# Kernel tuning notes

Measured on AMD Instinct MI355X. Metric: run time of the kernel, lower is better.

## Reference

```python
import jax, jax.numpy as jnp
import numpy as np

NUM_BINS = 32
FAIRNESS_PENALTY = 0.1
SENSITIVE = (0, 5)


def setup_inputs() -> dict:
    key = jax.random.key(0)
    k1, k2, k3, k4 = jax.random.split(key, 4)
    B, F, P = 65536, 256, 32
    x = jax.random.uniform(k1, (B, F), dtype=jnp.float32)  # features in [0,1)
    W = jax.random.normal(k2, (F, NUM_BINS), dtype=jnp.float32) * 0.1  # main-effect weights
    IW = jax.random.normal(k3, (P, NUM_BINS, NUM_BINS), dtype=jnp.float32) * 0.1  # pairwise weights
    intercept = jax.random.normal(k4, (1,), dtype=jnp.float32)
    # build(): feature_bins[i] = linspace(0, 1, num_bins+1) for every feature
    bins = jnp.tile(jnp.linspace(0.0, 1.0, NUM_BINS + 1, dtype=jnp.float32)[None, :], (F, 1))
    pair_i = jnp.arange(P, dtype=jnp.int32) * 2  # interaction_terms = [(0,1),(2,3),...]
    pair_j = pair_i + 1
    return dict(x=x, W=W, IW=IW, intercept=intercept, bins=bins, pair_i=pair_i, pair_j=pair_j)


def _bin_indices(x, bins):
    # x: [B,F], bins: [F,NB+1] -> int32 [B,F]; matches tf sum(x>=bins)-1 with clip
    idx = jnp.sum((x[:, :, None] >= bins[None, :, :]).astype(jnp.int32), axis=-1) - 1
    return jnp.clip(idx, 0, NUM_BINS - 1)


def reference(x, W, IW, intercept, bins, pair_i, pair_j):
    B, F = x.shape
    P = IW.shape[0]
    idx = _bin_indices(x, bins)  # [B,F]
    main = W[jnp.arange(F)[None, :], idx]  # per-feature gathered contributions [B,F]
    inter = IW[jnp.arange(P)[None, :], idx[:, pair_i], idx[:, pair_j]]  # [B,P]
    preds = intercept[0] + main.sum(axis=1) + inter.sum(axis=1)  # [B]
    fairness_loss = FAIRNESS_PENALTY * sum(jnp.var(main[:, s]) for s in SENSITIVE)
    return preds[:, None], fairness_loss
```

## Files before the change

### kernel.cpp

```cpp
#include <hip/hip_runtime.h>


#define F        256
#define NBINS    32
#define PPAIRS   32
#define WPB      8
#define BLOCK    (WPB * 64)
#define GRID     1024
#define WPAD     (NBINS + 1)

template <int ctrl, int row_mask, int bank_mask>
__device__ __forceinline__ float dpp_add(float x) {
    int y = __builtin_amdgcn_update_dpp(0, __float_as_int(x), ctrl, row_mask, bank_mask, false);
    return x + __int_as_float(y);
}

__device__ __forceinline__ float wave_sum_lane63(float x) {
    x = dpp_add<0x111, 0xf, 0xf>(x);
    x = dpp_add<0x112, 0xf, 0xf>(x);
    x = dpp_add<0x114, 0xf, 0xe>(x);
    x = dpp_add<0x118, 0xf, 0xc>(x);
    x = dpp_add<0x142, 0xa, 0xf>(x);
    x = dpp_add<0x143, 0x8, 0xf>(x);
    return x;
}

__global__ __launch_bounds__(BLOCK, 8) void febm_main(
    const float* __restrict__ x, const float* __restrict__ W,
    const float* __restrict__ IW, const float* __restrict__ intercept,
    float* __restrict__ out, float4* __restrict__ partials, int B)
{
    __shared__ float Wl[F * WPAD];
    __shared__ float4 mm[WPB];

    for (int i = threadIdx.x; i < F * NBINS; i += BLOCK) {
        int f = i >> 5, k = i & 31;
        Wl[f * WPAD + k] = W[i];
    }
    __syncthreads();

    const int lane = threadIdx.x & 63;
    const int wave = threadIdx.x >> 6;
    const int gw = blockIdx.x * WPB + wave;
    const int total_waves = GRID * WPB;
    const int rows_per_wave = B / total_waves;
    const int base = gw * rows_per_wave;

    const float c0 = intercept[0];

    float sA = 0.f, ssA = 0.f;

    const float4* xr = (const float4*)x;
    float4 xv = xr[(size_t)base * (F / 4) + lane];

    for (int r = 0; r < rows_per_wave; ++r) {
        const int b = base + r;
        float4 xnext;
        if (r + 1 < rows_per_wave)
            xnext = xr[(size_t)(b + 1) * (F / 4) + lane];

        float msum = 0.f, wf = 0.f;
        unsigned packed = 0;
        const float xe[4] = {xv.x, xv.y, xv.z, xv.w};
        #pragma unroll
        for (int i = 0; i < 4; ++i) {
            int k = (int)(xe[i] * 32.0f);
            k = k < 0 ? 0 : (k > NBINS - 1 ? NBINS - 1 : k);
            const int f = lane * 4 + i;
            const float w = Wl[f * WPAD + k];
            msum += w;
            packed |= (unsigned)k << (i * 8);
            if (i == 0) wf = w;
            if (i == 1 && lane == 1) wf = w;
        }

        const unsigned u = (unsigned)__shfl((int)packed, lane >> 1);
        float iv = 0.f;
        if (lane < PPAIRS) {
            const int sh = (lane & 1) * 16;
            const int ki = (u >> sh) & 0xff;
            const int kj = (u >> (sh + 8)) & 0xff;
            iv = IW[lane * (NBINS * NBINS) + ki * NBINS + kj];
        }

        const float tot = wave_sum_lane63(msum + iv);
        if (lane == 63) out[b] = c0 + tot;

        if (lane < 2) { sA += wf; ssA += wf * wf; }
        xv = xnext;
    }

    if (lane == 0) { mm[wave].x = sA; mm[wave].y = ssA; }
    if (lane == 1) { mm[wave].z = sA; mm[wave].w = ssA; }
    __syncthreads();
    if (threadIdx.x == 0) {
        float4 a = mm[0];
        #pragma unroll
        for (int w = 1; w < WPB; ++w) {
            a.x += mm[w].x; a.y += mm[w].y; a.z += mm[w].z; a.w += mm[w].w;
        }
        partials[blockIdx.x] = a;
    }
}

__global__ __launch_bounds__(256) void febm_reduce(
    const float4* __restrict__ partials, int nPart, float* __restrict__ fair_out, int B)
{
    __shared__ float4 sw[4];
    const int lane = threadIdx.x & 63;
    const int wave = threadIdx.x >> 6;

    float4 a = make_float4(0.f, 0.f, 0.f, 0.f);
    for (int i = threadIdx.x; i < nPart; i += 256) {
        const float4 p = partials[i];
        a.x += p.x; a.y += p.y; a.z += p.z; a.w += p.w;
    }
    #pragma unroll
    for (int off = 32; off > 0; off >>= 1) {
        a.x += __shfl_xor(a.x, off);
        a.y += __shfl_xor(a.y, off);
        a.z += __shfl_xor(a.z, off);
        a.w += __shfl_xor(a.w, off);
    }
    if (lane == 0) sw[wave] = a;
    __syncthreads();
    if (threadIdx.x == 0) {
        float4 t = sw[0];
        #pragma unroll
        for (int w = 1; w < 4; ++w) {
            t.x += sw[w].x; t.y += sw[w].y; t.z += sw[w].z; t.w += sw[w].w;
        }
        const double invB = 1.0 / (double)B;
        const double mean0 = t.x * invB, mean5 = t.z * invB;
        const double var0 = t.y * invB - mean0 * mean0;
        const double var5 = t.w * invB - mean5 * mean5;
        fair_out[0] = (float)(0.1 * (var0 + var5));
    }
}

extern "C" void kernel_launch(void* const* d_in, const int* in_sizes, int n_in,
                              void* d_out, int out_size, void* d_ws, size_t ws_size,
                              hipStream_t stream)
{
    const float* x         = (const float*)d_in[0];
    const float* W         = (const float*)d_in[1];
    const float* IW        = (const float*)d_in[2];
    const float* intercept = (const float*)d_in[3];

    float* out = (float*)d_out;
    const int B = in_sizes[0] / F;
    float4* partials = (float4*)d_ws;

    febm_main<<<GRID, BLOCK, 0, stream>>>(x, W, IW, intercept, out, partials, B);
    febm_reduce<<<1, 256, 0, stream>>>(partials, GRID, out + B, B);
}
```

Before: 116.9 us.

## Batch all per-wave row loads upfront and vectorize W staging and output stores

Each wave now issues all 8 of its row loads at once into registers, instead of a one-deep prefetch inside the loop. The per-row loop is fully unrolled with a fixed ROWS constant, and the 8 results are written as two float4 stores. W is staged into shared memory with float4 global loads, and the launch bound occupancy hint drops from 8 to 4. The aim is more memory-level parallelism for the 64 MB x stream, at the cost of higher register pressure. It also hardcodes B = GRID*WPB*ROWS, so other batch sizes would break.

```diff
diff --git a/kernel.cpp b/kernel.cpp
--- a/kernel.cpp
+++ b/kernel.cpp
@@ -7,6 +7,7 @@
 #define WPB      8
 #define BLOCK    (WPB * 64)
 #define GRID     1024
+#define ROWS     8
 #define WPAD     (NBINS + 1)
 
 template <int ctrl, int row_mask, int bank_mask>
@@ -25,69 +26,76 @@
     return x;
 }
 
-__global__ __launch_bounds__(BLOCK, 8) void febm_main(
+__global__ __launch_bounds__(BLOCK, 4) void febm_main(
     const float* __restrict__ x, const float* __restrict__ W,
     const float* __restrict__ IW, const float* __restrict__ intercept,
-    float* __restrict__ out, float4* __restrict__ partials, int B)
+    float* __restrict__ out, float4* __restrict__ partials)
 {
     __shared__ float Wl[F * WPAD];
     __shared__ float4 mm[WPB];
 
-    for (int i = threadIdx.x; i < F * NBINS; i += BLOCK) {
-        int f = i >> 5, k = i & 31;
-        Wl[f * WPAD + k] = W[i];
+    {
+        const float4* W4 = (const float4*)W;
+        for (int i = threadIdx.x; i < F * NBINS / 4; i += BLOCK) {
+            const float4 v = W4[i];
+            const int f = i >> 3, k4 = (i & 7) * 4;
+            float* dst = &Wl[f * WPAD + k4];
+            dst[0] = v.x; dst[1] = v.y; dst[2] = v.z; dst[3] = v.w;
+        }
     }
     __syncthreads();
 
     const int lane = threadIdx.x & 63;
     const int wave = threadIdx.x >> 6;
     const int gw = blockIdx.x * WPB + wave;
-    const int total_waves = GRID * WPB;
-    const int rows_per_wave = B / total_waves;
-    const int base = gw * rows_per_wave;
+    const int base = gw * ROWS;
 
     const float c0 = intercept[0];
 
+    const float4* xr = (const float4*)x;
+    float4 xv[ROWS];
+    #pragma unroll
+    for (int r = 0; r < ROWS; ++r)
+        xv[r] = xr[(size_t)(base + r) * (F / 4) + lane];
+
+    float msum[ROWS], iv[ROWS];
     float sA = 0.f, ssA = 0.f;
-
-    const float4* xr = (const float4*)x;
-    float4 xv = xr[(size_t)base * (F / 4) + lane];
-
-    for (int r = 0; r < rows_per_wave; ++r) {
-        const int b = base + r;
-        float4 xnext;
-        if (r + 1 < rows_per_wave)
-            xnext = xr[(size_t)(b + 1) * (F / 4) + lane];
-
-        float msum = 0.f, wf = 0.f;
+    #pragma unroll
+    for (int r = 0; r < ROWS; ++r) {
+        const float xe[4] = {xv[r].x, xv[r].y, xv[r].z, xv[r].w};
+        float acc = 0.f, wf = 0.f;
         unsigned packed = 0;
-        const float xe[4] = {xv.x, xv.y, xv.z, xv.w};
         #pragma unroll
         for (int i = 0; i < 4; ++i) {
             int k = (int)(xe[i] * 32.0f);
             k = k < 0 ? 0 : (k > NBINS - 1 ? NBINS - 1 : k);
-            const int f = lane * 4 + i;
-            const float w = Wl[f * WPAD + k];
-            msum += w;
+            const float w = Wl[(lane * 4 + i) * WPAD + k];
+            acc += w;
             packed |= (unsigned)k << (i * 8);
             if (i == 0) wf = w;
             if (i == 1 && lane == 1) wf = w;
         }
+        msum[r] = acc;
+        if (lane < 2) { sA += wf; ssA += wf * wf; }
 
         const unsigned u = (unsigned)__shfl((int)packed, lane >> 1);
-        float iv = 0.f;
+        float t = 0.f;
         if (lane < PPAIRS) {
             const int sh = (lane & 1) * 16;
             const int ki = (u >> sh) & 0xff;
             const int kj = (u >> (sh + 8)) & 0xff;
-            iv = IW[lane * (NBINS * NBINS) + ki * NBINS + kj];
+            t = IW[lane * (NBINS * NBINS) + ki * NBINS + kj];
         }
+        iv[r] = t;
+    }
 
-        const float tot = wave_sum_lane63(msum + iv);
-        if (lane == 63) out[b] = c0 + tot;
-
-        if (lane < 2) { sA += wf; ssA += wf * wf; }
-        xv = xnext;
+    float res[ROWS];
+    #pragma unroll
+    for (int r = 0; r < ROWS; ++r)
+        res[r] = c0 + wave_sum_lane63(msum[r] + iv[r]);
+    if (lane == 63) {
+        ((float4*)(out + base))[0] = make_float4(res[0], res[1], res[2], res[3]);
+        ((float4*)(out + base))[1] = make_float4(res[4], res[5], res[6], res[7]);
     }
 
     if (lane == 0) { mm[wave].x = sA; mm[wave].y = ssA; }
@@ -151,6 +159,6 @@
     const int B = in_sizes[0] / F;
     float4* partials = (float4*)d_ws;
 
-    febm_main<<<GRID, BLOCK, 0, stream>>>(x, W, IW, intercept, out, partials, B);
+    febm_main<<<GRID, BLOCK, 0, stream>>>(x, W, IW, intercept, out, partials);
     febm_reduce<<<1, 256, 0, stream>>>(partials, GRID, out + B, B);
 }
```

Result: faster. 111.9 us (-4.3%).
